# Kernel optimization log

Measured on AMD Instinct MI355X. Metric: run time of the kernel, lower is better.

## Reference

```python
import jax, jax.numpy as jnp
import numpy as np

D_MODEL = 768
KERNEL = 3

def setup_inputs() -> dict:
    key = jax.random.key(0)
    k1, k2 = jax.random.split(key)
    x = jax.random.normal(k1, (8, D_MODEL, 4096), dtype=jnp.float32)
    weight = jax.random.normal(k2, (D_MODEL, 1, KERNEL), dtype=jnp.float32)
    return {"x": x, "weight": weight}

def reference(x, weight):
    # Depthwise causal conv1d: pad left by k-1, no right pad -> output length == L,
    # identical to torch F.conv1d(pad=k-1) followed by y[..., :L].
    k = weight.shape[-1]
    y = jax.lax.conv_general_dilated(
        x, weight,
        window_strides=(1,),
        padding=[(k - 1, 0)],
        dimension_numbers=("NCH", "OIH", "NCH"),
        feature_group_count=x.shape[1],
    )
    return y
```

## Files before the change

### kernel.cpp

```cpp
#include <hip/hip_runtime.h>


#define CONV_L 4096
#define CONV_C 768

typedef float vfloat4 __attribute__((ext_vector_type(4)));

__global__ __launch_bounds__(256) void dwconv1d_k3_kernel(
    const float* __restrict__ x,
    const float* __restrict__ w,
    float* __restrict__ y)
{
    const int row = blockIdx.x >> 2;
    const int p4  = ((blockIdx.x & 3) << 8) + threadIdx.x;
    const int c   = row % CONV_C;

    const float w0 = w[c * 3 + 0];
    const float w1 = w[c * 3 + 1];
    const float w2 = w[c * 3 + 2];

    const float* xrow = x + (size_t)row * CONV_L;
    const float4 cur = ((const float4*)xrow)[p4];

    float xm1 = __shfl_up(cur.w, 1);
    float xm2 = __shfl_up(cur.z, 1);
    if ((threadIdx.x & 63) == 0) {
        if (p4 == 0) {
            xm1 = 0.0f; xm2 = 0.0f;
        } else {
            const float* xs = xrow + (p4 << 2);
            xm1 = xs[-1]; xm2 = xs[-2];
        }
    }

    vfloat4 out;
    out.x = w0 * xm2   + w1 * xm1   + w2 * cur.x;
    out.y = w0 * xm1   + w1 * cur.x + w2 * cur.y;
    out.z = w0 * cur.x + w1 * cur.y + w2 * cur.z;
    out.w = w0 * cur.y + w1 * cur.z + w2 * cur.w;

    __builtin_nontemporal_store(out,
        (vfloat4*)(y + (size_t)row * CONV_L + ((size_t)p4 << 2)));
}

extern "C" void kernel_launch(void* const* d_in, const int* in_sizes, int n_in,
                              void* d_out, int out_size, void* d_ws, size_t ws_size,
                              hipStream_t stream)
{
    const float* x = (const float*)d_in[0];
    const float* w = (const float*)d_in[1];
    float* y = (float*)d_out;

    const int rows = out_size / CONV_L;
    const int grid = rows * 4;
    dwconv1d_k3_kernel<<<grid, 256, 0, stream>>>(x, w, y);
}
```

Baseline: 172.1 us.

## Use grid-stride persistent loop with fixed grid for depthwise conv

Replaces the one-float4-per-thread launch of 24576 blocks with a fixed grid of 2048 blocks, each looping over flattened float4 indices with unroll 4. This is meant to cut block launch overhead and keep several loads in flight per thread. Every lane now loads the halo float2 unconditionally, the row index is made wave-uniform with readfirstlane, and the nontemporal store becomes a plain store, which may add cache pressure. The problem size is hardcoded into the launch instead of being derived from out_size.

```diff
diff --git a/kernel.cpp b/kernel.cpp
--- a/kernel.cpp
+++ b/kernel.cpp
@@ -1,46 +1,49 @@
 #include <hip/hip_runtime.h>
 
 
-#define CONV_L 4096
-#define CONV_C 768
+#define CONV_L   4096
+#define CONV_C   768
+#define N_F4     (8 * CONV_C * CONV_L / 4)
+#define THREADS  256
+#define BLOCKS   2048
+#define STRIDE   (BLOCKS * THREADS)
+#define ITERS    (N_F4 / STRIDE)
 
-typedef float vfloat4 __attribute__((ext_vector_type(4)));
-
-__global__ __launch_bounds__(256) void dwconv1d_k3_kernel(
+__global__ __launch_bounds__(THREADS) void dwconv1d_k3_flat(
     const float* __restrict__ x,
     const float* __restrict__ w,
     float* __restrict__ y)
 {
-    const int row = blockIdx.x >> 2;
-    const int p4  = ((blockIdx.x & 3) << 8) + threadIdx.x;
-    const int c   = row % CONV_C;
+    const int  tid  = blockIdx.x * THREADS + threadIdx.x;
+    const bool lead = (threadIdx.x & 63) == 0;
 
-    const float w0 = w[c * 3 + 0];
-    const float w1 = w[c * 3 + 1];
-    const float w2 = w[c * 3 + 2];
+#pragma unroll 4
+    for (int it = 0; it < ITERS; ++it) {
+        const int i = tid + it * STRIDE;
+        const float4 cur = ((const float4*)x)[i];
 
-    const float* xrow = x + (size_t)row * CONV_L;
-    const float4 cur = ((const float4*)xrow)[p4];
+        const int row = i >> 10;
+        const int c   = __builtin_amdgcn_readfirstlane(row) % CONV_C;
+        const float w0 = w[c * 3 + 0];
+        const float w1 = w[c * 3 + 1];
+        const float w2 = w[c * 3 + 2];
 
-    float xm1 = __shfl_up(cur.w, 1);
-    float xm2 = __shfl_up(cur.z, 1);
-    if ((threadIdx.x & 63) == 0) {
-        if (p4 == 0) {
-            xm1 = 0.0f; xm2 = 0.0f;
-        } else {
-            const float* xs = xrow + (p4 << 2);
-            xm1 = xs[-1]; xm2 = xs[-2];
-        }
+        const size_t f = ((size_t)i << 2);
+        const float2 h = *(const float2*)(x + (f ? f - 2 : 0));
+
+        float m1 = __shfl_up(cur.w, 1);
+        float m2 = __shfl_up(cur.z, 1);
+        if (lead)            { m2 = h.x;  m1 = h.y;  }
+        if ((i & 1023) == 0) { m2 = 0.0f; m1 = 0.0f; }
+
+        float4 o;
+        o.x = w0 * m2    + w1 * m1    + w2 * cur.x;
+        o.y = w0 * m1    + w1 * cur.x + w2 * cur.y;
+        o.z = w0 * cur.x + w1 * cur.y + w2 * cur.z;
+        o.w = w0 * cur.y + w1 * cur.z + w2 * cur.w;
+
+        ((float4*)y)[i] = o;
     }
-
-    vfloat4 out;
-    out.x = w0 * xm2   + w1 * xm1   + w2 * cur.x;
-    out.y = w0 * xm1   + w1 * cur.x + w2 * cur.y;
-    out.z = w0 * cur.x + w1 * cur.y + w2 * cur.z;
-    out.w = w0 * cur.y + w1 * cur.z + w2 * cur.w;
-
-    __builtin_nontemporal_store(out,
-        (vfloat4*)(y + (size_t)row * CONV_L + ((size_t)p4 << 2)));
 }
 
 extern "C" void kernel_launch(void* const* d_in, const int* in_sizes, int n_in,
@@ -50,8 +53,7 @@
     const float* x = (const float*)d_in[0];
     const float* w = (const float*)d_in[1];
     float* y = (float*)d_out;
+    (void)out_size;
 
-    const int rows = out_size / CONV_L;
-    const int grid = rows * 4;
-    dwconv1d_k3_kernel<<<grid, 256, 0, stream>>>(x, w, y);
+    dwconv1d_k3_flat<<<BLOCKS, THREADS, 0, stream>>>(x, w, y);
 }
```

Result: slower. 179.7 us (+4.4%).

## Stage each full row in LDS via direct global-to-LDS loads, one block per row

Applied to the files above, without the earlier changes.

Each block now handles one whole 4096-element row. It loads the row straight into shared memory with global_load_lds (16-byte) and computes the three-tap causal conv from LDS, which removes the wave shuffles and the extra global halo reads. It also drops the nontemporal store in favour of a normal store and cuts the grid by four, so each thread does four float4 outputs. The trade-offs are less parallelism per block, a full-row barrier before any compute, and 16KB of LDS per block, which may limit overlap in what is a purely bandwidth-bound kernel.

```diff
diff --git a/kernel.cpp b/kernel.cpp
--- a/kernel.cpp
+++ b/kernel.cpp
@@ -4,15 +4,14 @@
 #define CONV_L 4096
 #define CONV_C 768
 
-typedef float vfloat4 __attribute__((ext_vector_type(4)));
-
-__global__ __launch_bounds__(256) void dwconv1d_k3_kernel(
+__global__ __launch_bounds__(256) void dwconv1d_k3_lds(
     const float* __restrict__ x,
     const float* __restrict__ w,
     float* __restrict__ y)
 {
-    const int row = blockIdx.x >> 2;
-    const int p4  = ((blockIdx.x & 3) << 8) + threadIdx.x;
+    __shared__ __align__(16) float xs[CONV_L];
+
+    const int row = blockIdx.x;
     const int c   = row % CONV_C;
 
     const float w0 = w[c * 3 + 0];
@@ -20,27 +19,43 @@
     const float w2 = w[c * 3 + 2];
 
     const float* xrow = x + (size_t)row * CONV_L;
-    const float4 cur = ((const float4*)xrow)[p4];
+    float*       yrow = y + (size_t)row * CONV_L;
 
-    float xm1 = __shfl_up(cur.w, 1);
-    float xm2 = __shfl_up(cur.z, 1);
-    if ((threadIdx.x & 63) == 0) {
-        if (p4 == 0) {
-            xm1 = 0.0f; xm2 = 0.0f;
-        } else {
-            const float* xs = xrow + (p4 << 2);
-            xm1 = xs[-1]; xm2 = xs[-2];
-        }
+    const int t    = threadIdx.x;
+    const int wv   = t >> 6;
+    const int lane = t & 63;
+
+#pragma unroll
+    for (int k = 0; k < 4; ++k) {
+        const int chunk = (wv << 2) + k;
+        const float* src = xrow + (chunk << 8) + (lane << 2);
+        __builtin_amdgcn_global_load_lds(
+            (const __attribute__((address_space(1))) void*)src,
+            (__attribute__((address_space(3))) void*)&xs[chunk << 8],
+            16, 0, 0);
     }
+    __syncthreads();
 
-    vfloat4 out;
-    out.x = w0 * xm2   + w1 * xm1   + w2 * cur.x;
-    out.y = w0 * xm1   + w1 * cur.x + w2 * cur.y;
-    out.z = w0 * cur.x + w1 * cur.y + w2 * cur.z;
-    out.w = w0 * cur.y + w1 * cur.z + w2 * cur.w;
+    const float4* xs4  = (const float4*)xs;
+    float4*       yout = (float4*)yrow;
 
-    __builtin_nontemporal_store(out,
-        (vfloat4*)(y + (size_t)row * CONV_L + ((size_t)p4 << 2)));
+#pragma unroll
+    for (int s = 0; s < 4; ++s) {
+        const int f4 = t + (s << 8);
+        const float4 cur = xs4[f4];
+
+        const float2 h = *(const float2*)&xs[f4 ? ((f4 << 2) - 2) : 0];
+        const float m2 = f4 ? h.x : 0.0f;
+        const float m1 = f4 ? h.y : 0.0f;
+
+        float4 o;
+        o.x = w0 * m2    + w1 * m1    + w2 * cur.x;
+        o.y = w0 * m1    + w1 * cur.x + w2 * cur.y;
+        o.z = w0 * cur.x + w1 * cur.y + w2 * cur.z;
+        o.w = w0 * cur.y + w1 * cur.z + w2 * cur.w;
+
+        yout[f4] = o;
+    }
 }
 
 extern "C" void kernel_launch(void* const* d_in, const int* in_sizes, int n_in,
@@ -52,6 +67,5 @@
     float* y = (float*)d_out;
 
     const int rows = out_size / CONV_L;
-    const int grid = rows * 4;
-    dwconv1d_k3_kernel<<<grid, 256, 0, stream>>>(x, w, y);
+    dwconv1d_k3_lds<<<rows, 256, 0, stream>>>(x, w, y);
 }
```

Result: slower. 176.2 us (+2.4%).
